# Performance work log

Measured on AMD Instinct MI355X. Metric: run time of the kernel, lower is better.

## Reference

```python
import jax, jax.numpy as jnp
import numpy as np

EMBED_DIM = 512
NUM_HEADS = 8
HEAD_DIM = EMBED_DIM // NUM_HEADS
EDGE_HIDDEN = 512
B, L = 2, 512


def setup_inputs() -> dict:
    key = jax.random.key(0)
    ks = jax.random.split(key, 16)
    s = 0.02
    inp = {
        "query": jax.random.normal(ks[0], (B, L, EMBED_DIM), jnp.float32),
        "key_in": jax.random.normal(ks[1], (B, L, EMBED_DIM), jnp.float32),
        "value": jax.random.normal(ks[2], (B, L, EMBED_DIM), jnp.float32),
        "edge_representation": jax.random.normal(ks[3], (B, L, L), jnp.float32),
        # projection weights stored as [in, out]: y = x @ W + b
        "Wq": jax.random.normal(ks[4], (EMBED_DIM, EMBED_DIM), jnp.float32) * s,
        "bq": jnp.zeros((EMBED_DIM,), jnp.float32),
        "Wk": jax.random.normal(ks[5], (EMBED_DIM, EMBED_DIM), jnp.float32) * s,
        "bk": jnp.zeros((EMBED_DIM,), jnp.float32),
        "Wv": jax.random.normal(ks[6], (EMBED_DIM, EMBED_DIM), jnp.float32) * s,
        "bv": jnp.zeros((EMBED_DIM,), jnp.float32),
        "Wo": jax.random.normal(ks[7], (EMBED_DIM, EMBED_DIM), jnp.float32) * s,
        "bo": jnp.zeros((EMBED_DIM,), jnp.float32),
        # edge MLP: Linear(1 -> 512) -> ReLU -> Linear(512 -> num_heads)
        "We1": jax.random.normal(ks[8], (1, EDGE_HIDDEN), jnp.float32) * s,
        "be1": jnp.zeros((EDGE_HIDDEN,), jnp.float32),
        "We2": jax.random.normal(ks[9], (EDGE_HIDDEN, NUM_HEADS), jnp.float32) * s,
        "be2": jnp.zeros((NUM_HEADS,), jnp.float32),
    }
    return inp


def reference(query, key_in, value, edge_representation,
              Wq, bq, Wk, bk, Wv, bv, Wo, bo, We1, be1, We2, be2):
    Bc, Lc, _ = query.shape
    # project and split heads: [B, H, L, Dh]
    def split_heads(x):
        return x.reshape(Bc, Lc, NUM_HEADS, HEAD_DIM).transpose(0, 2, 1, 3)
    Q = split_heads(query @ Wq + bq)
    K = split_heads(key_in @ Wk + bk)
    V = split_heads(value @ Wv + bv)
    # edge MLP on scalar edge features: [B, L, L, 1] -> [B, L, L, H]
    e = edge_representation[..., None]
    h = jax.nn.relu(e * We1[0] + be1)          # [B, L, L, 512]
    edge_bias = h @ We2 + be2                   # [B, L, L, H]
    scale = 1.0 / jnp.sqrt(jnp.asarray(HEAD_DIM, query.dtype))
    scores = jnp.einsum("bhqd,bhkd->bhqk", Q, K) * scale
    scores = scores + edge_bias.transpose(0, 3, 1, 2)  # [B, H, L, L]
    attn = jax.nn.softmax(scores, axis=-1)
    out = jnp.einsum("bhqk,bhkd->bhqd", attn, V)
    out = out.transpose(0, 2, 1, 3).reshape(Bc, Lc, EMBED_DIM)
    return out @ Wo + bo
```

## Files before the change

kernel.cpp:

```cpp
#include <hip/hip_runtime.h>
#include <hip/hip_bf16.h>

typedef __attribute__((ext_vector_type(8))) short bf16x8;
typedef __attribute__((ext_vector_type(4))) float f32x4;

#define LOG2E 1.44269504088896340736f

#define XQ_OFF 0
#define XK_OFF 524288
#define XV_OFF 1048576
#define WQ_OFF 1572864
#define WK_OFF 1835008
#define WV_OFF 2097152
#define WO_OFF 2359296
#define QB_OFF 2621440
#define KB_OFF 3145728
#define VT_OFF 3670016
#define AO_OFF 4194304
#define T_B   9437184
#define A_B   (T_B + 4096)
#define C_B   (A_B + 20480)
#define SEG_B (C_B + 20480)

__device__ __forceinline__ unsigned short f2bf(float f) {
  union { __hip_bfloat16 h; unsigned short u; } c;
  c.h = __float2bfloat16(f);
  return c.u;
}

__global__ __launch_bounds__(512) void k_prep(
    const float* __restrict__ w1, const float* __restrict__ b1,
    const float* __restrict__ we2, const float* __restrict__ be2,
    float* __restrict__ wsT, float* __restrict__ wsA, float* __restrict__ wsC) {
  __shared__ float sT[512];
  __shared__ int sIdx[512];
  __shared__ float sDA[512][8];
  __shared__ float sDC[512][8];
  __shared__ float sA0[8], sC0[8];
  int tid = threadIdx.x;
  float w = w1[tid], bb = b1[tid];
  sT[tid] = (w != 0.f) ? (-bb / w) : -3.4e38f;
  sIdx[tid] = tid;
  {
#pragma unroll
    for (int h = 0; h < 8; ++h) {
      float w2 = we2[tid * 8 + h];
      float ra = 0.f, rc = 0.f;
      if (w < 0.f)       { ra = w2 * w; rc = w2 * bb; }
      else if (w == 0.f) { rc = w2 * fmaxf(bb, 0.f); }
      sDA[tid][h] = ra; sDC[tid][h] = rc;
    }
  }
  for (int size = 2; size <= 512; size <<= 1) {
    for (int stride = size >> 1; stride > 0; stride >>= 1) {
      __syncthreads();
      int i = tid, j = tid ^ stride;
      if (j > i) {
        bool up = ((i & size) == 0);
        float ti = sT[i], tj = sT[j];
        if (up ? (ti > tj) : (ti < tj)) {
          sT[i] = tj; sT[j] = ti;
          int t = sIdx[i]; sIdx[i] = sIdx[j]; sIdx[j] = t;
        }
      }
    }
  }
  for (int st = 256; st > 0; st >>= 1) {
    __syncthreads();
    if (tid < st) {
#pragma unroll
      for (int h = 0; h < 8; ++h) { sDA[tid][h] += sDA[tid + st][h]; sDC[tid][h] += sDC[tid + st][h]; }
    }
  }
  __syncthreads();
  if (tid < 8) { sA0[tid] = sDA[0][tid]; sC0[tid] = sDC[0][tid] + be2[tid]; }
  __syncthreads();
  {
    int k = sIdx[tid];
    float wk = w1[k], bk = b1[k];
#pragma unroll
    for (int h = 0; h < 8; ++h) {
      float w2 = we2[k * 8 + h];
      float da = 0.f, dc = 0.f;
      if (wk > 0.f)      { da =  w2 * wk; dc =  w2 * bk; }
      else if (wk < 0.f) { da = -w2 * wk; dc = -w2 * bk; }
      sDA[tid][h] = da; sDC[tid][h] = dc;
    }
  }
  __syncthreads();
  for (int off = 1; off < 512; off <<= 1) {
    float ta[8], tc[8];
    bool act = (tid >= off);
    if (act) {
#pragma unroll
      for (int h = 0; h < 8; ++h) { ta[h] = sDA[tid - off][h]; tc[h] = sDC[tid - off][h]; }
    }
    __syncthreads();
    if (act) {
#pragma unroll
      for (int h = 0; h < 8; ++h) { sDA[tid][h] += ta[h]; sDC[tid][h] += tc[h]; }
    }
    __syncthreads();
  }
  wsT[tid] = sT[tid];
  if (tid < 8) { wsA[tid] = sA0[tid]; wsC[tid] = sC0[tid]; }
#pragma unroll
  for (int h = 0; h < 8; ++h) {
    wsA[(tid + 1) * 8 + h] = sA0[h] + sDA[tid][h];
    wsC[(tid + 1) * 8 + h] = sC0[h] + sDC[tid][h];
  }
}

__global__ __launch_bounds__(256) void k_pre(
    const float* __restrict__ xq, const float* __restrict__ xk, const float* __restrict__ xv,
    const float* __restrict__ wq, const float* __restrict__ wk, const float* __restrict__ wv,
    const float* __restrict__ wo, const float* __restrict__ eg,
    const float* __restrict__ wsT, unsigned short* __restrict__ wsb,
    unsigned short* __restrict__ segp) {
  __shared__ __align__(16) char smem[64 * 68 * 2];
  int blk = blockIdx.x, tid = threadIdx.x;
  if (blk < 256) {
    unsigned short (*sWt)[68] = (unsigned short (*)[68])smem;
    int mat = blk >> 6, tile = blk & 63;
    int k0 = (tile >> 3) * 64, n0 = (tile & 7) * 64;
    const float* src = (mat == 0) ? wq : (mat == 1) ? wk : (mat == 2) ? wv : wo;
    int row = tid >> 2, cq = tid & 3;
    const float4* sp = (const float4*)(src + (size_t)(k0 + row) * 512 + n0 + cq * 16);
#pragma unroll
    for (int j = 0; j < 4; ++j) {
      float4 v = sp[j];
      int nl = cq * 16 + j * 4;
      sWt[nl + 0][row] = f2bf(v.x);
      sWt[nl + 1][row] = f2bf(v.y);
      sWt[nl + 2][row] = f2bf(v.z);
      sWt[nl + 3][row] = f2bf(v.w);
    }
    __syncthreads();
    int n = tid >> 2, kq = tid & 3;
    unsigned short* dst = wsb + WQ_OFF + mat * 262144 + (size_t)(n0 + n) * 512 + k0 + kq * 16;
    *(uint4*)dst       = *(const uint4*)&sWt[n][kq * 16];
    *(uint4*)(dst + 8) = *(const uint4*)&sWt[n][kq * 16 + 8];
  } else if (blk < 1792) {
    int i = (blk - 256) * 256 + tid;
    int region = i >> 17;
    int off = i & 131071;
    const float* src = (region == 0) ? xq : (region == 1) ? xk : xv;
    float4 v = ((const float4*)src)[off];
    ushort4 o;
    o.x = f2bf(v.x); o.y = f2bf(v.y); o.z = f2bf(v.z); o.w = f2bf(v.w);
    ((ushort4*)wsb)[i] = o;
  } else {
    float* sT = (float*)smem;
    sT[tid] = wsT[tid];
    sT[tid + 256] = wsT[tid + 256];
    __syncthreads();
    int i = (blk - 1792) * 256 + tid;
    float ev = eg[i];
    int lo = 0, hi = 512;
    while (lo < hi) {
      int mid = (lo + hi) >> 1;
      if (sT[mid] < ev) lo = mid + 1; else hi = mid;
    }
    segp[i] = (unsigned short)lo;
  }
}

struct GemmBatch {
  const unsigned short* A;
  const unsigned short* Wt;
  const float* bias;
  void* out;
  int mode;
};

__global__ __launch_bounds__(256) void k_gemm(GemmBatch g0, GemmBatch g1, GemmBatch g2) {
  GemmBatch g = (blockIdx.z == 0) ? g0 : (blockIdx.z == 1) ? g1 : g2;
  const int K = 512;
  int m0 = blockIdx.x * 64, n0 = blockIdx.y * 64;
  int tid = threadIdx.x, wave = tid >> 6, lane = tid & 63;
  int quad = lane >> 4, l16 = lane & 15;
  __shared__ __align__(16) unsigned short sA[64][72];
  __shared__ __align__(16) unsigned short sBt[64][72];
  f32x4 acc[4] = {{0.f,0.f,0.f,0.f},{0.f,0.f,0.f,0.f},{0.f,0.f,0.f,0.f},{0.f,0.f,0.f,0.f}};
  int lr = tid >> 2, ls = tid & 3;
  for (int kb = 0; kb < K; kb += 64) {
    __syncthreads();
    *(uint4*)&sA[lr][ls * 16]      = *(const uint4*)(g.A  + (size_t)(m0 + lr) * K + kb + ls * 16);
    *(uint4*)&sA[lr][ls * 16 + 8]  = *(const uint4*)(g.A  + (size_t)(m0 + lr) * K + kb + ls * 16 + 8);
    *(uint4*)&sBt[lr][ls * 16]     = *(const uint4*)(g.Wt + (size_t)(n0 + lr) * K + kb + ls * 16);
    *(uint4*)&sBt[lr][ls * 16 + 8] = *(const uint4*)(g.Wt + (size_t)(n0 + lr) * K + kb + ls * 16 + 8);
    __syncthreads();
    for (int ks = 0; ks < 2; ++ks) {
      bf16x8 af = *(const bf16x8*)&sA[wave * 16 + l16][ks * 32 + quad * 8];
      for (int nt = 0; nt < 4; ++nt) {
        bf16x8 bf = *(const bf16x8*)&sBt[nt * 16 + l16][ks * 32 + quad * 8];
        acc[nt] = __builtin_amdgcn_mfma_f32_16x16x32_bf16(af, bf, acc[nt], 0, 0, 0);
      }
    }
  }
  int mbase = m0 + wave * 16 + quad * 4;
  for (int nt = 0; nt < 4; ++nt) {
    int n = n0 + nt * 16 + l16;
    float bv = g.bias[n];
    for (int r = 0; r < 4; ++r) {
      float v = acc[nt][r] + bv;
      int m = mbase + r;
      if (g.mode == 0) {
        int b = m >> 9, l = m & 511, hh = n >> 6, d = n & 63;
        ((unsigned short*)g.out)[(((size_t)(b * 8 + hh) * 512) + l) * 64 + d] = f2bf(v);
      } else if (g.mode == 1) {
        ((float*)g.out)[(size_t)m * 512 + n] = v;
      } else {
        int b = m >> 9, l = m & 511, hh = n >> 6, d = n & 63;
        ((unsigned short*)g.out)[(((size_t)(b * 8 + hh) * 64) + d) * 512 + l] = f2bf(v);
      }
    }
  }
}

__global__ __launch_bounds__(256) void k_attn(
    const unsigned short* __restrict__ Qb, const unsigned short* __restrict__ Kb,
    const unsigned short* __restrict__ Vt, const float* __restrict__ eg,
    const unsigned short* __restrict__ segp,
    const float* __restrict__ wsA, const float* __restrict__ wsC,
    unsigned short* __restrict__ ao) {
  int qt = blockIdx.x, h = blockIdx.y, b = blockIdx.z;
  int bh = b * 8 + h;
  int q0 = qt * 16;
  int tid = threadIdx.x, wave = tid >> 6, lane = tid & 63;
  int quad = lane >> 4, l16 = lane & 15;
  __shared__ float sAh[513], sCh[513];
  __shared__ __align__(16) unsigned short sP[4][16][36];
  __shared__ float sO[4][4][16][16];
  __shared__ float sM[4][16], sL[4][16];
  for (int i = tid; i < 513; i += 256) { sAh[i] = wsA[i * 8 + h]; sCh[i] = wsC[i * 8 + h]; }
  const unsigned short* qp = Qb + ((size_t)bh * 512 + q0 + l16) * 64 + quad * 8;
  bf16x8 qf0 = *(const bf16x8*)qp;
  bf16x8 qf1 = *(const bf16x8*)(qp + 32);
  int key_base = wave * 128;
  f32x4 S[4][2];
#pragma unroll
  for (int kt = 0; kt < 4; ++kt) {
    int key0 = key_base + kt * 32;
#pragma unroll
    for (int half = 0; half < 2; ++half) {
      const unsigned short* kp = Kb + ((size_t)bh * 512 + key0 + half * 16 + l16) * 64 + quad * 8;
      bf16x8 kf0 = *(const bf16x8*)kp;
      bf16x8 kf1 = *(const bf16x8*)(kp + 32);
      f32x4 acc = {0.f, 0.f, 0.f, 0.f};
      acc = __builtin_amdgcn_mfma_f32_16x16x32_bf16(qf0, kf0, acc, 0, 0, 0);
      acc = __builtin_amdgcn_mfma_f32_16x16x32_bf16(qf1, kf1, acc, 0, 0, 0);
      S[kt][half] = acc;
    }
  }
  __syncthreads();
#pragma unroll
  for (int kt = 0; kt < 4; ++kt)
#pragma unroll
    for (int half = 0; half < 2; ++half)
#pragma unroll
      for (int r = 0; r < 4; ++r) {
        int eidx = (b * 512 + q0 + quad * 4 + r) * 512 + key_base + kt * 32 + half * 16 + l16;
        float ev = eg[eidx];
        int sg = segp[eidx];
        S[kt][half][r] = S[kt][half][r] * 0.125f + sAh[sg] * ev + sCh[sg];
      }
  float m_w[4], l_w[4];
#pragma unroll
  for (int r = 0; r < 4; ++r) {
    float mx = -3.4e38f;
#pragma unroll
    for (int kt = 0; kt < 4; ++kt) { mx = fmaxf(mx, fmaxf(S[kt][0][r], S[kt][1][r])); }
    for (int off = 1; off < 16; off <<= 1) mx = fmaxf(mx, __shfl_xor(mx, off, 64));
    float s = 0.f;
#pragma unroll
    for (int kt = 0; kt < 4; ++kt)
#pragma unroll
      for (int half = 0; half < 2; ++half) {
        float p = exp2f((S[kt][half][r] - mx) * LOG2E);
        S[kt][half][r] = p; s += p;
      }
    for (int off = 1; off < 16; off <<= 1) s += __shfl_xor(s, off, 64);
    m_w[r] = mx; l_w[r] = s;
  }
  f32x4 Oacc[4] = {{0.f,0.f,0.f,0.f},{0.f,0.f,0.f,0.f},{0.f,0.f,0.f,0.f},{0.f,0.f,0.f,0.f}};
#pragma unroll
  for (int kt = 0; kt < 4; ++kt) {
    int key0 = key_base + kt * 32;
#pragma unroll
    for (int half = 0; half < 2; ++half)
#pragma unroll
      for (int r = 0; r < 4; ++r)
        sP[wave][quad * 4 + r][half * 16 + l16] = f2bf(S[kt][half][r]);
    __builtin_amdgcn_wave_barrier();
    bf16x8 pf = *(const bf16x8*)&sP[wave][l16][quad * 8];
    __builtin_amdgcn_wave_barrier();
#pragma unroll
    for (int nt = 0; nt < 4; ++nt) {
      bf16x8 vf = *(const bf16x8*)(Vt + ((size_t)bh * 64 + nt * 16 + l16) * 512 + key0 + quad * 8);
      Oacc[nt] = __builtin_amdgcn_mfma_f32_16x16x32_bf16(pf, vf, Oacc[nt], 0, 0, 0);
    }
  }
  if (l16 == 0) {
#pragma unroll
    for (int r = 0; r < 4; ++r) { sM[wave][quad * 4 + r] = m_w[r]; sL[wave][quad * 4 + r] = l_w[r]; }
  }
#pragma unroll
  for (int nt = 0; nt < 4; ++nt)
#pragma unroll
    for (int r = 0; r < 4; ++r)
      sO[wave][nt][quad * 4 + r][l16] = Oacc[nt][r];
  __syncthreads();
#pragma unroll
  for (int r = 0; r < 4; ++r) {
    int row = quad * 4 + r;
    float M = fmaxf(fmaxf(sM[0][row], sM[1][row]), fmaxf(sM[2][row], sM[3][row]));
    float L = 0.f, Ov = 0.f;
#pragma unroll
    for (int wv = 0; wv < 4; ++wv) {
      float f = exp2f((sM[wv][row] - M) * LOG2E);
      L += f * sL[wv][row];
      Ov += f * sO[wv][wave][row][l16];
    }
    float v = Ov / L;
    ao[((size_t)(b * 512 + q0 + row)) * 512 + h * 64 + wave * 16 + l16] = f2bf(v);
  }
}

extern "C" void kernel_launch(void* const* d_in, const int* in_sizes, int n_in,
                              void* d_out, int out_size, void* d_ws, size_t ws_size,
                              hipStream_t stream) {
  const float* q   = (const float*)d_in[0];
  const float* kin = (const float*)d_in[1];
  const float* v   = (const float*)d_in[2];
  const float* eg  = (const float*)d_in[3];
  const float* Wq  = (const float*)d_in[4];
  const float* bq  = (const float*)d_in[5];
  const float* Wk  = (const float*)d_in[6];
  const float* bk  = (const float*)d_in[7];
  const float* Wv  = (const float*)d_in[8];
  const float* bv  = (const float*)d_in[9];
  const float* Wo  = (const float*)d_in[10];
  const float* bo  = (const float*)d_in[11];
  const float* We1 = (const float*)d_in[12];
  const float* be1 = (const float*)d_in[13];
  const float* We2 = (const float*)d_in[14];
  const float* be2 = (const float*)d_in[15];
  unsigned short* wsb = (unsigned short*)d_ws;
  float* wsT = (float*)((char*)d_ws + T_B);
  float* wsA = (float*)((char*)d_ws + A_B);
  float* wsC = (float*)((char*)d_ws + C_B);
  unsigned short* segp = (unsigned short*)((char*)d_ws + SEG_B);

  k_prep<<<1, 512, 0, stream>>>(We1, be1, We2, be2, wsT, wsA, wsC);
  k_pre<<<3840, 256, 0, stream>>>(q, kin, v, Wq, Wk, Wv, Wo, eg, wsT, wsb, segp);
  GemmBatch gq{wsb + XQ_OFF, wsb + WQ_OFF, bq, (void*)(wsb + QB_OFF), 0};
  GemmBatch gk{wsb + XK_OFF, wsb + WK_OFF, bk, (void*)(wsb + KB_OFF), 0};
  GemmBatch gv{wsb + XV_OFF, wsb + WV_OFF, bv, (void*)(wsb + VT_OFF), 2};
  k_gemm<<<dim3(16, 8, 3), 256, 0, stream>>>(gq, gk, gv);
  k_attn<<<dim3(32, 8, 2), 256, 0, stream>>>(wsb + QB_OFF, wsb + KB_OFF, wsb + VT_OFF,
                                             eg, segp, wsA, wsC, wsb + AO_OFF);
  GemmBatch go{wsb + AO_OFF, wsb + WO_OFF, bo, d_out, 1};
  k_gemm<<<dim3(16, 8, 1), 256, 0, stream>>>(go, go, go);
}
```

Baseline: 141.6 us.

## Fuse all stages into one cooperative persistent kernel with grid syncs

Replaces the five separate launches (prep, preprocessing, QKV GEMM, attention, output GEMM) with a single cooperative kernel of 512 blocks that runs each stage as a phase separated by grid-wide syncs. The seg search is moved into the same phase as the QKV GEMM so it can overlap. The prep stage is re-mapped onto 256 threads. The goal is to remove launch overheads and inter-kernel gaps, at the cost of grid.sync barriers and a prep phase that runs on only one block while the others do conversions. A fallback path with four ordinary launches is kept in case the cooperative launch fails.

```diff
diff --git a/kernel.cpp b/kernel.cpp
--- a/kernel.cpp
+++ b/kernel.cpp
@@ -1,5 +1,8 @@
 #include <hip/hip_runtime.h>
 #include <hip/hip_bf16.h>
+#include <hip/hip_cooperative_groups.h>
+
+namespace cg = cooperative_groups;
 
 typedef __attribute__((ext_vector_type(8))) short bf16x8;
 typedef __attribute__((ext_vector_type(4))) float f32x4;
@@ -22,114 +25,133 @@
 #define C_B   (A_B + 20480)
 #define SEG_B (C_B + 20480)
 
+#define SMEM_BYTES 37120
+
+struct MegaArgs {
+  const float *xq, *xk, *xv, *eg;
+  const float *wq, *wk, *wv, *wo;
+  const float *bq, *bk, *bv, *bo;
+  const float *w1, *b1, *we2, *be2;
+  float* out;
+  unsigned short* wsb;
+  float *wsT, *wsA, *wsC;
+  unsigned short* segp;
+};
+
 __device__ __forceinline__ unsigned short f2bf(float f) {
   union { __hip_bfloat16 h; unsigned short u; } c;
   c.h = __float2bfloat16(f);
   return c.u;
 }
 
-__global__ __launch_bounds__(512) void k_prep(
-    const float* __restrict__ w1, const float* __restrict__ b1,
-    const float* __restrict__ we2, const float* __restrict__ be2,
-    float* __restrict__ wsT, float* __restrict__ wsA, float* __restrict__ wsC) {
-  __shared__ float sT[512];
-  __shared__ int sIdx[512];
-  __shared__ float sDA[512][8];
-  __shared__ float sDC[512][8];
-  __shared__ float sA0[8], sC0[8];
+__device__ void prep_block(const MegaArgs& a, char* smem) {
+  float* sT   = (float*)smem;
+  int*   sIdx = (int*)(smem + 2048);
+  float (*sDA)[8] = (float (*)[8])(smem + 4096);
+  float (*sDC)[8] = (float (*)[8])(smem + 20480);
+  float* sA0 = (float*)(smem + 36864);
+  float* sC0 = (float*)(smem + 36896);
   int tid = threadIdx.x;
-  float w = w1[tid], bb = b1[tid];
-  sT[tid] = (w != 0.f) ? (-bb / w) : -3.4e38f;
-  sIdx[tid] = tid;
-  {
+  for (int p = tid; p < 512; p += 256) {
+    float w = a.w1[p], bb = a.b1[p];
+    sT[p] = (w != 0.f) ? (-bb / w) : -3.4e38f;
+    sIdx[p] = p;
 #pragma unroll
     for (int h = 0; h < 8; ++h) {
-      float w2 = we2[tid * 8 + h];
+      float w2 = a.we2[p * 8 + h];
       float ra = 0.f, rc = 0.f;
       if (w < 0.f)       { ra = w2 * w; rc = w2 * bb; }
       else if (w == 0.f) { rc = w2 * fmaxf(bb, 0.f); }
-      sDA[tid][h] = ra; sDC[tid][h] = rc;
-    }
-  }
+      sDA[p][h] = ra; sDC[p][h] = rc;
+    }
+  }
+  __syncthreads();
   for (int size = 2; size <= 512; size <<= 1) {
     for (int stride = size >> 1; stride > 0; stride >>= 1) {
+      int p = tid;
+      int i = ((p / stride) * (stride << 1)) + (p % stride);
+      int j = i + stride;
+      bool up = ((i & size) == 0);
+      float ti = sT[i], tj = sT[j];
+      if (up ? (ti > tj) : (ti < tj)) {
+        sT[i] = tj; sT[j] = ti;
+        int t = sIdx[i]; sIdx[i] = sIdx[j]; sIdx[j] = t;
+      }
       __syncthreads();
-      int i = tid, j = tid ^ stride;
-      if (j > i) {
-        bool up = ((i & size) == 0);
-        float ti = sT[i], tj = sT[j];
-        if (up ? (ti > tj) : (ti < tj)) {
-          sT[i] = tj; sT[j] = ti;
-          int t = sIdx[i]; sIdx[i] = sIdx[j]; sIdx[j] = t;
-        }
-      }
-    }
-  }
-  for (int st = 256; st > 0; st >>= 1) {
-    __syncthreads();
+    }
+  }
+#pragma unroll
+  for (int h = 0; h < 8; ++h) { sDA[tid][h] += sDA[tid + 256][h]; sDC[tid][h] += sDC[tid + 256][h]; }
+  __syncthreads();
+  for (int st = 128; st > 0; st >>= 1) {
     if (tid < st) {
 #pragma unroll
       for (int h = 0; h < 8; ++h) { sDA[tid][h] += sDA[tid + st][h]; sDC[tid][h] += sDC[tid + st][h]; }
     }
-  }
-  __syncthreads();
-  if (tid < 8) { sA0[tid] = sDA[0][tid]; sC0[tid] = sDC[0][tid] + be2[tid]; }
-  __syncthreads();
-  {
-    int k = sIdx[tid];
-    float wk = w1[k], bk = b1[k];
+    __syncthreads();
+  }
+  if (tid < 8) { sA0[tid] = sDA[0][tid]; sC0[tid] = sDC[0][tid] + a.be2[tid]; }
+  __syncthreads();
+  for (int p = tid; p < 512; p += 256) {
+    int k = sIdx[p];
+    float wk = a.w1[k], bk2 = a.b1[k];
 #pragma unroll
     for (int h = 0; h < 8; ++h) {
-      float w2 = we2[k * 8 + h];
+      float w2 = a.we2[k * 8 + h];
       float da = 0.f, dc = 0.f;
-      if (wk > 0.f)      { da =  w2 * wk; dc =  w2 * bk; }
-      else if (wk < 0.f) { da = -w2 * wk; dc = -w2 * bk; }
-      sDA[tid][h] = da; sDC[tid][h] = dc;
+      if (wk > 0.f)      { da =  w2 * wk; dc =  w2 * bk2; }
+      else if (wk < 0.f) { da = -w2 * wk; dc = -w2 * bk2; }
+      sDA[p][h] = da; sDC[p][h] = dc;
     }
   }
   __syncthreads();
   for (int off = 1; off < 512; off <<= 1) {
-    float ta[8], tc[8];
-    bool act = (tid >= off);
-    if (act) {
-#pragma unroll
-      for (int h = 0; h < 8; ++h) { ta[h] = sDA[tid - off][h]; tc[h] = sDC[tid - off][h]; }
-    }
-    __syncthreads();
-    if (act) {
-#pragma unroll
-      for (int h = 0; h < 8; ++h) { sDA[tid][h] += ta[h]; sDC[tid][h] += tc[h]; }
-    }
-    __syncthreads();
-  }
-  wsT[tid] = sT[tid];
-  if (tid < 8) { wsA[tid] = sA0[tid]; wsC[tid] = sC0[tid]; }
-#pragma unroll
-  for (int h = 0; h < 8; ++h) {
-    wsA[(tid + 1) * 8 + h] = sA0[h] + sDA[tid][h];
-    wsC[(tid + 1) * 8 + h] = sC0[h] + sDC[tid][h];
-  }
-}
-
-__global__ __launch_bounds__(256) void k_pre(
-    const float* __restrict__ xq, const float* __restrict__ xk, const float* __restrict__ xv,
-    const float* __restrict__ wq, const float* __restrict__ wk, const float* __restrict__ wv,
-    const float* __restrict__ wo, const float* __restrict__ eg,
-    const float* __restrict__ wsT, unsigned short* __restrict__ wsb,
-    unsigned short* __restrict__ segp) {
-  __shared__ __align__(16) char smem[64 * 68 * 2];
-  int blk = blockIdx.x, tid = threadIdx.x;
-  if (blk < 256) {
-    unsigned short (*sWt)[68] = (unsigned short (*)[68])smem;
-    int mat = blk >> 6, tile = blk & 63;
+    float ra[2][8], rc[2][8];
+#pragma unroll
+    for (int e = 0; e < 2; ++e) {
+      int p = tid + e * 256;
+      if (p >= off) {
+#pragma unroll
+        for (int h = 0; h < 8; ++h) { ra[e][h] = sDA[p - off][h]; rc[e][h] = sDC[p - off][h]; }
+      }
+    }
+    __syncthreads();
+#pragma unroll
+    for (int e = 0; e < 2; ++e) {
+      int p = tid + e * 256;
+      if (p >= off) {
+#pragma unroll
+        for (int h = 0; h < 8; ++h) { sDA[p][h] += ra[e][h]; sDC[p][h] += rc[e][h]; }
+      }
+    }
+    __syncthreads();
+  }
+  a.wsT[tid] = sT[tid]; a.wsT[tid + 256] = sT[tid + 256];
+  if (tid < 8) { a.wsA[tid] = sA0[tid]; a.wsC[tid] = sC0[tid]; }
+  for (int p = tid; p < 512; p += 256) {
+#pragma unroll
+    for (int h = 0; h < 8; ++h) {
+      a.wsA[(p + 1) * 8 + h] = sA0[h] + sDA[p][h];
+      a.wsC[(p + 1) * 8 + h] = sC0[h] + sDC[p][h];
+    }
+  }
+}
+
+__device__ void transpose2(const MegaArgs& a, int tblk, char* smem) {
+  unsigned short (*sWt)[72] = (unsigned short (*)[72])smem;
+  int tid = threadIdx.x;
+  for (int it = 0; it < 2; ++it) {
+    int t = tblk * 2 + it;
+    int mat = t >> 6, tile = t & 63;
     int k0 = (tile >> 3) * 64, n0 = (tile & 7) * 64;
-    const float* src = (mat == 0) ? wq : (mat == 1) ? wk : (mat == 2) ? wv : wo;
+    const float* src = (mat == 0) ? a.wq : (mat == 1) ? a.wk : (mat == 2) ? a.wv : a.wo;
     int row = tid >> 2, cq = tid & 3;
     const float4* sp = (const float4*)(src + (size_t)(k0 + row) * 512 + n0 + cq * 16);
-#pragma unroll
-    for (int j = 0; j < 4; ++j) {
-      float4 v = sp[j];
-      int nl = cq * 16 + j * 4;
+    if (it) __syncthreads();
+#pragma unroll
+    for (int j2 = 0; j2 < 4; ++j2) {
+      float4 v = sp[j2];
+      int nl = cq * 16 + j2 * 4;
       sWt[nl + 0][row] = f2bf(v.x);
       sWt[nl + 1][row] = f2bf(v.y);
       sWt[nl + 2][row] = f2bf(v.z);
@@ -137,103 +159,107 @@
     }
     __syncthreads();
     int n = tid >> 2, kq = tid & 3;
-    unsigned short* dst = wsb + WQ_OFF + mat * 262144 + (size_t)(n0 + n) * 512 + k0 + kq * 16;
+    unsigned short* dst = a.wsb + WQ_OFF + mat * 262144 + (size_t)(n0 + n) * 512 + k0 + kq * 16;
     *(uint4*)dst       = *(const uint4*)&sWt[n][kq * 16];
     *(uint4*)(dst + 8) = *(const uint4*)&sWt[n][kq * 16 + 8];
-  } else if (blk < 1792) {
-    int i = (blk - 256) * 256 + tid;
-    int region = i >> 17;
-    int off = i & 131071;
-    const float* src = (region == 0) ? xq : (region == 1) ? xk : xv;
+  }
+}
+
+__device__ void convert_units(const MegaArgs& a, int blk) {
+  int tid = threadIdx.x;
+  for (int u = blk - 129; u < 1536; u += 383) {
+    int i = u * 256 + tid;
+    int region = i >> 17, off = i & 131071;
+    const float* src = (region == 0) ? a.xq : (region == 1) ? a.xk : a.xv;
     float4 v = ((const float4*)src)[off];
     ushort4 o;
     o.x = f2bf(v.x); o.y = f2bf(v.y); o.z = f2bf(v.z); o.w = f2bf(v.w);
-    ((ushort4*)wsb)[i] = o;
-  } else {
-    float* sT = (float*)smem;
-    sT[tid] = wsT[tid];
-    sT[tid + 256] = wsT[tid + 256];
-    __syncthreads();
-    int i = (blk - 1792) * 256 + tid;
-    float ev = eg[i];
+    ((ushort4*)a.wsb)[i] = o;
+  }
+}
+
+__device__ void seg_block(const MegaArgs& a, int sblk, char* smem) {
+  float* sT = (float*)smem;
+  int tid = threadIdx.x;
+  sT[tid] = a.wsT[tid]; sT[tid + 256] = a.wsT[tid + 256];
+  __syncthreads();
+  int base = sblk * 4096;
+  for (int j2 = 0; j2 < 16; ++j2) {
+    int i = base + j2 * 256 + tid;
+    float ev = a.eg[i];
     int lo = 0, hi = 512;
     while (lo < hi) {
       int mid = (lo + hi) >> 1;
       if (sT[mid] < ev) lo = mid + 1; else hi = mid;
     }
-    segp[i] = (unsigned short)lo;
-  }
-}
-
-struct GemmBatch {
-  const unsigned short* A;
-  const unsigned short* Wt;
-  const float* bias;
-  void* out;
-  int mode;
-};
-
-__global__ __launch_bounds__(256) void k_gemm(GemmBatch g0, GemmBatch g1, GemmBatch g2) {
-  GemmBatch g = (blockIdx.z == 0) ? g0 : (blockIdx.z == 1) ? g1 : g2;
+    a.segp[i] = (unsigned short)lo;
+  }
+}
+
+__device__ void gemm_tile(const unsigned short* __restrict__ A, const unsigned short* __restrict__ Wt,
+                          const float* __restrict__ bias, void* out, int mode,
+                          int m0, int n0, char* smem) {
   const int K = 512;
-  int m0 = blockIdx.x * 64, n0 = blockIdx.y * 64;
+  unsigned short (*sA)[72]  = (unsigned short (*)[72])smem;
+  unsigned short (*sBt)[72] = (unsigned short (*)[72])(smem + 9216);
   int tid = threadIdx.x, wave = tid >> 6, lane = tid & 63;
   int quad = lane >> 4, l16 = lane & 15;
-  __shared__ __align__(16) unsigned short sA[64][72];
-  __shared__ __align__(16) unsigned short sBt[64][72];
   f32x4 acc[4] = {{0.f,0.f,0.f,0.f},{0.f,0.f,0.f,0.f},{0.f,0.f,0.f,0.f},{0.f,0.f,0.f,0.f}};
   int lr = tid >> 2, ls = tid & 3;
   for (int kb = 0; kb < K; kb += 64) {
     __syncthreads();
-    *(uint4*)&sA[lr][ls * 16]      = *(const uint4*)(g.A  + (size_t)(m0 + lr) * K + kb + ls * 16);
-    *(uint4*)&sA[lr][ls * 16 + 8]  = *(const uint4*)(g.A  + (size_t)(m0 + lr) * K + kb + ls * 16 + 8);
-    *(uint4*)&sBt[lr][ls * 16]     = *(const uint4*)(g.Wt + (size_t)(n0 + lr) * K + kb + ls * 16);
-    *(uint4*)&sBt[lr][ls * 16 + 8] = *(const uint4*)(g.Wt + (size_t)(n0 + lr) * K + kb + ls * 16 + 8);
+    *(uint4*)&sA[lr][ls * 16]      = *(const uint4*)(A  + (size_t)(m0 + lr) * K + kb + ls * 16);
+    *(uint4*)&sA[lr][ls * 16 + 8]  = *(const uint4*)(A  + (size_t)(m0 + lr) * K + kb + ls * 16 + 8);
+    *(uint4*)&sBt[lr][ls * 16]     = *(const uint4*)(Wt + (size_t)(n0 + lr) * K + kb + ls * 16);
+    *(uint4*)&sBt[lr][ls * 16 + 8] = *(const uint4*)(Wt + (size_t)(n0 + lr) * K + kb + ls * 16 + 8);
     __syncthreads();
     for (int ks = 0; ks < 2; ++ks) {
       bf16x8 af = *(const bf16x8*)&sA[wave * 16 + l16][ks * 32 + quad * 8];
+#pragma unroll
       for (int nt = 0; nt < 4; ++nt) {
         bf16x8 bf = *(const bf16x8*)&sBt[nt * 16 + l16][ks * 32 + quad * 8];
         acc[nt] = __builtin_amdgcn_mfma_f32_16x16x32_bf16(af, bf, acc[nt], 0, 0, 0);
       }
     }
   }
+  __syncthreads();
   int mbase = m0 + wave * 16 + quad * 4;
+#pragma unroll
   for (int nt = 0; nt < 4; ++nt) {
     int n = n0 + nt * 16 + l16;
-    float bv = g.bias[n];
+    float bv = bias[n];
+#pragma unroll
     for (int r = 0; r < 4; ++r) {
       float v = acc[nt][r] + bv;
       int m = mbase + r;
-      if (g.mode == 0) {
+      if (mode == 0) {
         int b = m >> 9, l = m & 511, hh = n >> 6, d = n & 63;
-        ((unsigned short*)g.out)[(((size_t)(b * 8 + hh) * 512) + l) * 64 + d] = f2bf(v);
-      } else if (g.mode == 1) {
-        ((float*)g.out)[(size_t)m * 512 + n] = v;
+        ((unsigned short*)out)[(((size_t)(b * 8 + hh) * 512) + l) * 64 + d] = f2bf(v);
+      } else if (mode == 1) {
+        ((float*)out)[(size_t)m * 512 + n] = v;
       } else {
         int b = m >> 9, l = m & 511, hh = n >> 6, d = n & 63;
-        ((unsigned short*)g.out)[(((size_t)(b * 8 + hh) * 64) + d) * 512 + l] = f2bf(v);
-      }
-    }
-  }
-}
-
-__global__ __launch_bounds__(256) void k_attn(
-    const unsigned short* __restrict__ Qb, const unsigned short* __restrict__ Kb,
-    const unsigned short* __restrict__ Vt, const float* __restrict__ eg,
-    const unsigned short* __restrict__ segp,
-    const float* __restrict__ wsA, const float* __restrict__ wsC,
-    unsigned short* __restrict__ ao) {
-  int qt = blockIdx.x, h = blockIdx.y, b = blockIdx.z;
+        ((unsigned short*)out)[(((size_t)(b * 8 + hh) * 64) + d) * 512 + l] = f2bf(v);
+      }
+    }
+  }
+}
+
+__device__ void attn_block(const MegaArgs& a, int qt, int h, int b, char* smem) {
+  float* sAh = (float*)smem;
+  float* sCh = (float*)(smem + 2052);
+  unsigned short (*sP)[16][40] = (unsigned short (*)[16][40])(smem + 4112);
+  float (*sO)[4][16][16] = (float (*)[4][16][16])(smem + 9232);
+  float (*sM)[16] = (float (*)[16])(smem + 25616);
+  float (*sL)[16] = (float (*)[16])(smem + 25872);
+  const unsigned short* Qb = a.wsb + QB_OFF;
+  const unsigned short* Kb = a.wsb + KB_OFF;
+  const unsigned short* Vt = a.wsb + VT_OFF;
   int bh = b * 8 + h;
   int q0 = qt * 16;
   int tid = threadIdx.x, wave = tid >> 6, lane = tid & 63;
   int quad = lane >> 4, l16 = lane & 15;
-  __shared__ float sAh[513], sCh[513];
-  __shared__ __align__(16) unsigned short sP[4][16][36];
-  __shared__ float sO[4][4][16][16];
-  __shared__ float sM[4][16], sL[4][16];
-  for (int i = tid; i < 513; i += 256) { sAh[i] = wsA[i * 8 + h]; sCh[i] = wsC[i * 8 + h]; }
+  for (int i = tid; i < 513; i += 256) { sAh[i] = a.wsA[i * 8 + h]; sCh[i] = a.wsC[i * 8 + h]; }
   const unsigned short* qp = Qb + ((size_t)bh * 512 + q0 + l16) * 64 + quad * 8;
   bf16x8 qf0 = *(const bf16x8*)qp;
   bf16x8 qf1 = *(const bf16x8*)(qp + 32);
@@ -261,8 +287,8 @@
 #pragma unroll
       for (int r = 0; r < 4; ++r) {
         int eidx = (b * 512 + q0 + quad * 4 + r) * 512 + key_base + kt * 32 + half * 16 + l16;
-        float ev = eg[eidx];
-        int sg = segp[eidx];
+        float ev = a.eg[eidx];
+        int sg = a.segp[eidx];
         S[kt][half][r] = S[kt][half][r] * 0.125f + sAh[sg] * ev + sCh[sg];
       }
   float m_w[4], l_w[4];
@@ -323,43 +349,97 @@
       Ov += f * sO[wv][wave][row][l16];
     }
     float v = Ov / L;
-    ao[((size_t)(b * 512 + q0 + row)) * 512 + h * 64 + wave * 16 + l16] = f2bf(v);
-  }
+    (a.wsb + AO_OFF)[((size_t)(b * 512 + q0 + row)) * 512 + h * 64 + wave * 16 + l16] = f2bf(v);
+  }
+}
+
+__device__ void phase0(const MegaArgs& a, int blk, char* smem) {
+  if (blk == 0) prep_block(a, smem);
+  else if (blk <= 128) transpose2(a, blk - 1, smem);
+  else convert_units(a, blk);
+}
+__device__ void phase1(const MegaArgs& a, int blk, char* smem) {
+  if (blk < 384) {
+    int z = blk >> 7, rem = blk & 127;
+    const unsigned short* A  = a.wsb + ((z == 0) ? XQ_OFF : (z == 1) ? XK_OFF : XV_OFF);
+    const unsigned short* Wt = a.wsb + ((z == 0) ? WQ_OFF : (z == 1) ? WK_OFF : WV_OFF);
+    const float* bias = (z == 0) ? a.bq : (z == 1) ? a.bk : a.bv;
+    void* outp = (void*)(a.wsb + ((z == 0) ? QB_OFF : (z == 1) ? KB_OFF : VT_OFF));
+    gemm_tile(A, Wt, bias, outp, (z == 2) ? 2 : 0, (rem & 15) * 64, (rem >> 4) * 64, smem);
+  } else {
+    seg_block(a, blk - 384, smem);
+  }
+}
+
+__global__ __launch_bounds__(256) void k_mega(MegaArgs a) {
+  cg::grid_group grid = cg::this_grid();
+  __shared__ __align__(16) char smem[SMEM_BYTES];
+  int blk = blockIdx.x;
+  phase0(a, blk, smem);
+  grid.sync();
+  phase1(a, blk, smem);
+  grid.sync();
+  attn_block(a, blk & 31, (blk >> 5) & 7, blk >> 8, smem);
+  grid.sync();
+  if (blk < 128)
+    gemm_tile(a.wsb + AO_OFF, a.wsb + WO_OFF, a.bo, (void*)a.out, 1,
+              (blk & 15) * 64, (blk >> 4) * 64, smem);
+}
+
+__global__ __launch_bounds__(256) void fb_p0(MegaArgs a) {
+  __shared__ __align__(16) char smem[SMEM_BYTES];
+  phase0(a, blockIdx.x, smem);
+}
+__global__ __launch_bounds__(256) void fb_p1(MegaArgs a) {
+  __shared__ __align__(16) char smem[SMEM_BYTES];
+  phase1(a, blockIdx.x, smem);
+}
+__global__ __launch_bounds__(256) void fb_p2(MegaArgs a) {
+  __shared__ __align__(16) char smem[SMEM_BYTES];
+  int blk = blockIdx.x;
+  attn_block(a, blk & 31, (blk >> 5) & 7, blk >> 8, smem);
+}
+__global__ __launch_bounds__(256) void fb_p3(MegaArgs a) {
+  __shared__ __align__(16) char smem[SMEM_BYTES];
+  gemm_tile(a.wsb + AO_OFF, a.wsb + WO_OFF, a.bo, (void*)a.out, 1,
+            (blockIdx.x & 15) * 64, (blockIdx.x >> 4) * 64, smem);
 }
 
 extern "C" void kernel_launch(void* const* d_in, const int* in_sizes, int n_in,
                               void* d_out, int out_size, void* d_ws, size_t ws_size,
                               hipStream_t stream) {
-  const float* q   = (const float*)d_in[0];
-  const float* kin = (const float*)d_in[1];
-  const float* v   = (const float*)d_in[2];
-  const float* eg  = (const float*)d_in[3];
-  const float* Wq  = (const float*)d_in[4];
-  const float* bq  = (const float*)d_in[5];
-  const float* Wk  = (const float*)d_in[6];
-  const float* bk  = (const float*)d_in[7];
-  const float* Wv  = (const float*)d_in[8];
-  const float* bv  = (const float*)d_in[9];
-  const float* Wo  = (const float*)d_in[10];
-  const float* bo  = (const float*)d_in[11];
-  const float* We1 = (const float*)d_in[12];
-  const float* be1 = (const float*)d_in[13];
-  const float* We2 = (const float*)d_in[14];
-  const float* be2 = (const float*)d_in[15];
-  unsigned short* wsb = (unsigned short*)d_ws;
-  float* wsT = (float*)((char*)d_ws + T_B);
-  float* wsA = (float*)((char*)d_ws + A_B);
-  float* wsC = (float*)((char*)d_ws + C_B);
-  unsigned short* segp = (unsigned short*)((char*)d_ws + SEG_B);
-
-  k_prep<<<1, 512, 0, stream>>>(We1, be1, We2, be2, wsT, wsA, wsC);
-  k_pre<<<3840, 256, 0, stream>>>(q, kin, v, Wq, Wk, Wv, Wo, eg, wsT, wsb, segp);
-  GemmBatch gq{wsb + XQ_OFF, wsb + WQ_OFF, bq, (void*)(wsb + QB_OFF), 0};
-  GemmBatch gk{wsb + XK_OFF, wsb + WK_OFF, bk, (void*)(wsb + KB_OFF), 0};
-  GemmBatch gv{wsb + XV_OFF, wsb + WV_OFF, bv, (void*)(wsb + VT_OFF), 2};
-  k_gemm<<<dim3(16, 8, 3), 256, 0, stream>>>(gq, gk, gv);
-  k_attn<<<dim3(32, 8, 2), 256, 0, stream>>>(wsb + QB_OFF, wsb + KB_OFF, wsb + VT_OFF,
-                                             eg, segp, wsA, wsC, wsb + AO_OFF);
-  GemmBatch go{wsb + AO_OFF, wsb + WO_OFF, bo, d_out, 1};
-  k_gemm<<<dim3(16, 8, 1), 256, 0, stream>>>(go, go, go);
-}
+  MegaArgs a;
+  a.xq  = (const float*)d_in[0];
+  a.xk  = (const float*)d_in[1];
+  a.xv  = (const float*)d_in[2];
+  a.eg  = (const float*)d_in[3];
+  a.wq  = (const float*)d_in[4];
+  a.bq  = (const float*)d_in[5];
+  a.wk  = (const float*)d_in[6];
+  a.bk  = (const float*)d_in[7];
+  a.wv  = (const float*)d_in[8];
+  a.bv  = (const float*)d_in[9];
+  a.wo  = (const float*)d_in[10];
+  a.bo  = (const float*)d_in[11];
+  a.w1  = (const float*)d_in[12];
+  a.b1  = (const float*)d_in[13];
+  a.we2 = (const float*)d_in[14];
+  a.be2 = (const float*)d_in[15];
+  a.out = (float*)d_out;
+  a.wsb = (unsigned short*)d_ws;
+  a.wsT = (float*)((char*)d_ws + T_B);
+  a.wsA = (float*)((char*)d_ws + A_B);
+  a.wsC = (float*)((char*)d_ws + C_B);
+  a.segp = (unsigned short*)((char*)d_ws + SEG_B);
+
+  void* kargs[] = { (void*)&a };
+  hipError_t err = hipLaunchCooperativeKernel((const void*)k_mega, dim3(512), dim3(256),
+                                              kargs, 0, stream);
+  if (err != hipSuccess) {
+    (void)hipGetLastError();
+    fb_p0<<<512, 256, 0, stream>>>(a);
+    fb_p1<<<512, 256, 0, stream>>>(a);
+    fb_p2<<<512, 256, 0, stream>>>(a);
+    fb_p3<<<128, 256, 0, stream>>>(a);
+  }
+}
```

After: 359.9 us. 154% more time.
